# Kernel tuning notes

Hardware: AMD Instinct MI355X
Metric: run time of the kernel (lower is better)

Reference implementation:

```python
import jax, jax.numpy as jnp
import numpy as np

DIM = 1024
HEADS = 16
HEAD_DIM = DIM // HEADS


def setup_inputs() -> dict:
    key = jax.random.key(0)
    ks = jax.random.split(key, 10)
    B, N, M = 4, 2048, 2048
    s = 1.0 / np.sqrt(DIM)
    return {
        "x": jax.random.normal(ks[0], (B, N, DIM), jnp.float32),
        "context": jax.random.normal(ks[1], (B, M, DIM), jnp.float32),
        "Wq": jax.random.normal(ks[2], (DIM, DIM), jnp.float32) * s,
        "bq": jnp.zeros((DIM,), jnp.float32),
        "Wk": jax.random.normal(ks[3], (DIM, DIM), jnp.float32) * s,
        "bk": jnp.zeros((DIM,), jnp.float32),
        "Wv": jax.random.normal(ks[4], (DIM, DIM), jnp.float32) * s,
        "bv": jnp.zeros((DIM,), jnp.float32),
        "Wo": jax.random.normal(ks[5], (DIM, DIM), jnp.float32) * s,
        "bo": jnp.zeros((DIM,), jnp.float32),
    }


def reference(x, context, Wq, bq, Wk, bk, Wv, bv, Wo, bo):
    B, N, C = x.shape
    M = context.shape[1]
    scale = HEAD_DIM ** (-0.5)
    # projections + split heads: [B, H, L, D]
    q = (x @ Wq.T + bq).reshape(B, N, HEADS, HEAD_DIM).transpose(0, 2, 1, 3)
    k = (context @ Wk.T + bk).reshape(B, M, HEADS, HEAD_DIM).transpose(0, 2, 1, 3)
    v = (context @ Wv.T + bv).reshape(B, M, HEADS, HEAD_DIM).transpose(0, 2, 1, 3)
    attn = jax.nn.softmax(jnp.einsum('bhnd,bhmd->bhnm', q, k) * scale, axis=-1)
    out = jnp.einsum('bhnm,bhmd->bhnd', attn, v)  # [B, H, N, D]
    out = out.transpose(0, 2, 1, 3).reshape(B, N, C)
    return out @ Wo.T + bo
```

## Files before the change

kernel.cpp:

```cpp
#include <hip/hip_runtime.h>
#include <hip/hip_bf16.h>
#include <stdint.h>


#define HEADS 16
#define HD 64
#define NSEQ 2048
#define DIMSZ 1024

typedef __bf16 bf16x8_t __attribute__((ext_vector_type(8)));
typedef float f32x4_t __attribute__((ext_vector_type(4)));
typedef short s16x4 __attribute__((ext_vector_type(4)));
typedef unsigned short u16;
typedef unsigned int u32;

__device__ __forceinline__ u16 f2bf(float f) {
    union { float f; u32 i; } x; x.f = f;
    u32 r = x.i + 0x7FFF + ((x.i >> 16) & 1);
    return (u16)(r >> 16);
}
__device__ __forceinline__ u32 pk2(float a, float b) {
    __hip_bfloat162 h = __float22bfloat162_rn(float2{a, b});
    union { __hip_bfloat162 h2; u32 u; } c; c.h2 = h; return c.u;
}

__device__ __forceinline__ void pl32swap(u32& a, u32& b) {
    asm("v_permlane32_swap_b32 %0, %1" : "+v"(a), "+v"(b));
}
__device__ __forceinline__ void pl16swap(u32& a, u32& b) {
    asm("v_permlane16_swap_b32 %0, %1" : "+v"(a), "+v"(b));
}

#define GLDS(g, l) __builtin_amdgcn_global_load_lds( \
    (const __attribute__((address_space(1))) void*)(g), \
    (__attribute__((address_space(3))) void*)(l), 16, 0, 0)

__global__ __launch_bounds__(256)
void cvt_all(const float* __restrict__ x, const float* __restrict__ ctx,
             const float* __restrict__ wq, const float* __restrict__ wk,
             const float* __restrict__ wv, const float* __restrict__ wo,
             u16* __restrict__ xb, u16* __restrict__ ctxb,
             u16* __restrict__ wqb, u16* __restrict__ wkb,
             u16* __restrict__ wvb, u16* __restrict__ wob)
{
    long g = (long)blockIdx.x * 256 + threadIdx.x;
    const float* in; u16* out; long off;
    if (g < 1048576L)      { in = x;   out = xb;   off = g; }
    else if (g < 2097152L) { in = ctx; out = ctxb; off = g - 1048576L; }
    else if (g < 2228224L) { in = wq;  out = wqb;  off = g - 2097152L; }
    else if (g < 2359296L) { in = wk;  out = wkb;  off = g - 2228224L; }
    else if (g < 2490368L) { in = wv;  out = wvb;  off = g - 2359296L; }
    else                   { in = wo;  out = wob;  off = g - 2490368L; }
    long i = off * 8;
    float4 a = *(const float4*)(in + i);
    float4 b = *(const float4*)(in + i + 4);
    union { uint4 v; u16 h[8]; } u;
    u.h[0] = f2bf(a.x); u.h[1] = f2bf(a.y); u.h[2] = f2bf(a.z); u.h[3] = f2bf(a.w);
    u.h[4] = f2bf(b.x); u.h[5] = f2bf(b.y); u.h[6] = f2bf(b.z); u.h[7] = f2bf(b.w);
    *(uint4*)(out + i) = u.v;
}

#define BM 128
#define BN 128

#define BKQ 64

__global__ __launch_bounds__(256, 3)
void qkv_gemm(const u16* __restrict__ xb, const u16* __restrict__ ctxb,
              const u16* __restrict__ wq, const u16* __restrict__ wk,
              const u16* __restrict__ wv,
              const float* __restrict__ bq, const float* __restrict__ bk,
              const float* __restrict__ bv,
              u16* __restrict__ qo, u16* __restrict__ ko, u16* __restrict__ vo,
              float qscale)
{
    __shared__ __align__(16) u16 Asm[BM * BKQ];
    __shared__ __align__(16) u16 Wsm[BN * BKQ];

    const int g    = blockIdx.x >> 3;
    const int col0 = (blockIdx.x & 7) * BN;
    const int row0 = blockIdx.y * BM;

    const u16* A = (g == 0) ? xb : ctxb;
    const u16* W = (g == 0) ? wq : (g == 1) ? wk : wv;
    const float* bias = (g == 0) ? bq : (g == 1) ? bk : bv;
    const float scale = (g == 0) ? qscale : 1.0f;

    const int t    = threadIdx.x;
    const int lane = t & 63;
    const int wid  = t >> 6;
    const int lrow = lane & 15;
    const int lq   = lane >> 4;
    const int wm   = (wid >> 1) * 64;
    const int wn   = (wid & 1) * 64;

    const u16* gA[4]; const u16* gW[4];
    u16* lA[4]; u16* lW[4];
    #pragma unroll
    for (int q = 0; q < 4; q++) {
        int s = q * 256 + t;
        int r = s >> 3;
        int c = (s & 7) ^ (r & 7);
        gA[q] = A + (long)(row0 + r) * DIMSZ + c * 8;
        gW[q] = W + (long)(col0 + r) * DIMSZ + c * 8;
        int lofs = (q * 256 + wid * 64) * 8;
        lA[q] = &Asm[lofs];
        lW[q] = &Wsm[lofs];
    }

    f32x4_t zero = {0.f, 0.f, 0.f, 0.f};
    f32x4_t acc[4][4];
    #pragma unroll
    for (int i = 0; i < 4; i++)
        #pragma unroll
        for (int j = 0; j < 4; j++) acc[i][j] = zero;

    const int rsw = lrow & 7;

    for (int k0 = 0; k0 < DIMSZ; k0 += BKQ) {
        __syncthreads();
        #pragma unroll
        for (int q = 0; q < 4; q++) {
            GLDS(gA[q] + k0, lA[q]);
            GLDS(gW[q] + k0, lW[q]);
        }
        __syncthreads();

        #pragma unroll
        for (int kk = 0; kk < 2; kk++) {
            bf16x8_t af[4], bfr[4];
            #pragma unroll
            for (int i = 0; i < 4; i++)
                af[i] = *(const bf16x8_t*)
                    &Asm[(wm + 16 * i + lrow) * BKQ + (((kk * 4 + lq) ^ rsw) << 3)];
            #pragma unroll
            for (int j = 0; j < 4; j++)
                bfr[j] = *(const bf16x8_t*)
                    &Wsm[(wn + 16 * j + lrow) * BKQ + (((kk * 4 + lq) ^ rsw) << 3)];
            #pragma unroll
            for (int i = 0; i < 4; i++)
                #pragma unroll
                for (int j = 0; j < 4; j++)
                    acc[i][j] = __builtin_amdgcn_mfma_f32_16x16x32_bf16(
                        af[i], bfr[j], acc[i][j], 0, 0, 0);
        }
    }

    float bvv[4];
    #pragma unroll
    for (int j = 0; j < 4; j++) bvv[j] = bias[col0 + wn + 16 * j + lrow];

    if (g < 2) {
        u16* out = g ? ko : qo;
        #pragma unroll
        for (int i = 0; i < 4; i++) {
            #pragma unroll
            for (int j = 0; j < 4; j++) {
                int cc = col0 + wn + 16 * j + lrow;
                #pragma unroll
                for (int r = 0; r < 4; r++) {
                    int rr = row0 + wm + 16 * i + lq * 4 + r;
                    float v = (acc[i][j][r] + bvv[j]) * scale;
                    int b = rr >> 11, n = rr & 2047;
                    int h = cc >> 6,  d = cc & 63;
                    long oidx = ((long)((b * HEADS + h) * NSEQ + n) << 6) + d;
                    out[oidx] = f2bf(v);
                }
            }
        }
    } else {
        #pragma unroll
        for (int i = 0; i < 4; i++) {
            int n0 = row0 + wm + 16 * i + lq * 4;
            int b  = n0 >> 11, nn = n0 & 2047;
            #pragma unroll
            for (int j = 0; j < 4; j++) {
                int d = col0 + wn + 16 * j + lrow;
                uint2 p;
                p.x = pk2(acc[i][j][0] + bvv[j], acc[i][j][1] + bvv[j]);
                p.y = pk2(acc[i][j][2] + bvv[j], acc[i][j][3] + bvv[j]);
                long o = ((long)((b * HEADS + (d >> 6)) * HD + (d & 63)) << 11) + nn;
                *(uint2*)&vo[o] = p;
            }
        }
    }
}

#define BMO 64
#define BKO 64

__global__ __launch_bounds__(256, 4)
void gemm_o(const u16* __restrict__ A, const u16* __restrict__ W,
            const float* __restrict__ bias, float* __restrict__ out)
{
    __shared__ __align__(16) u16 Asm[BMO * BKO];
    __shared__ __align__(16) u16 Wsm[BN * BKO];

    const int t    = threadIdx.x;
    const int lane = t & 63;
    const int wid  = t >> 6;
    const int lrow = lane & 15;
    const int lq   = lane >> 4;
    const int wm   = (wid >> 1) * 32;
    const int wn   = (wid & 1) * 64;
    const int row0 = blockIdx.y * BMO;
    const int col0 = blockIdx.x * BN;

    const u16* gA[2]; u16* lA[2];
    #pragma unroll
    for (int q = 0; q < 2; q++) {
        int s = q * 256 + t;
        int r = s >> 3;
        int c = (s & 7) ^ (r & 7);
        gA[q] = A + (long)(row0 + r) * DIMSZ + c * 8;
        lA[q] = &Asm[(q * 256 + wid * 64) * 8];
    }
    const u16* gW[4]; u16* lW[4];
    #pragma unroll
    for (int q = 0; q < 4; q++) {
        int s = q * 256 + t;
        int r = s >> 3;
        int c = (s & 7) ^ (r & 7);
        gW[q] = W + (long)(col0 + r) * DIMSZ + c * 8;
        lW[q] = &Wsm[(q * 256 + wid * 64) * 8];
    }

    f32x4_t zero = {0.f, 0.f, 0.f, 0.f};
    f32x4_t acc[2][4];
    #pragma unroll
    for (int i = 0; i < 2; i++)
        #pragma unroll
        for (int j = 0; j < 4; j++) acc[i][j] = zero;

    const int rsw = lrow & 7;

    for (int k0 = 0; k0 < DIMSZ; k0 += BKO) {
        __syncthreads();
        GLDS(gA[0] + k0, lA[0]);
        GLDS(gA[1] + k0, lA[1]);
        #pragma unroll
        for (int q = 0; q < 4; q++) GLDS(gW[q] + k0, lW[q]);
        __syncthreads();

        #pragma unroll
        for (int kk = 0; kk < 2; kk++) {
            bf16x8_t af[2], bfr[4];
            #pragma unroll
            for (int i = 0; i < 2; i++)
                af[i] = *(const bf16x8_t*)
                    &Asm[(wm + 16 * i + lrow) * BKO + (((kk * 4 + lq) ^ rsw) << 3)];
            #pragma unroll
            for (int j = 0; j < 4; j++)
                bfr[j] = *(const bf16x8_t*)
                    &Wsm[(wn + 16 * j + lrow) * BKO + (((kk * 4 + lq) ^ rsw) << 3)];
            #pragma unroll
            for (int i = 0; i < 2; i++)
                #pragma unroll
                for (int j = 0; j < 4; j++)
                    acc[i][j] = __builtin_amdgcn_mfma_f32_16x16x32_bf16(
                        af[i], bfr[j], acc[i][j], 0, 0, 0);
        }
    }

    float bvv[4];
    #pragma unroll
    for (int j = 0; j < 4; j++) bvv[j] = bias[col0 + wn + 16 * j + lrow];

    #pragma unroll
    for (int i = 0; i < 2; i++) {
        #pragma unroll
        for (int j = 0; j < 4; j++) {
            int cc = col0 + wn + 16 * j + lrow;
            #pragma unroll
            for (int r = 0; r < 4; r++) {
                int rr = row0 + wm + 16 * i + lq * 4 + r;
                out[(long)rr * DIMSZ + cc] = acc[i][j][r] + bvv[j];
            }
        }
    }
}

__global__ __launch_bounds__(256, 4)
void attn(const u16* __restrict__ Q, const u16* __restrict__ K,
          const u16* __restrict__ Vt, u16* __restrict__ O)
{
    __shared__ __align__(16) u16 Ksm[2][64 * 64];
    __shared__ __align__(16) u16 Vsm[2][64 * 64];

    const int t    = threadIdx.x;
    const int lane = t & 63;
    const int w    = t >> 6;
    const int lrow = lane & 15;
    const int lq   = lane >> 4;
    const int bh   = blockIdx.x;
    const int q0   = blockIdx.y * 128;
    const int b    = bh >> 4;
    const int h    = bh & 15;

    bf16x8_t qf[2][2];
    #pragma unroll
    for (int qa = 0; qa < 2; qa++) {
        const long qbase = ((long)bh * NSEQ + q0 + w * 32 + qa * 16 + lrow) * HD;
        qf[qa][0] = *(const bf16x8_t*)&Q[qbase + lq * 8];
        qf[qa][1] = *(const bf16x8_t*)&Q[qbase + lq * 8 + 32];
    }

    const long kvbase = (long)bh * NSEQ * HD;

    const u16* gK[2]; const u16* gV[2]; int lofs[2];
    #pragma unroll
    for (int c = 0; c < 2; c++) {
        int s  = c * 256 + t;
        int r  = s >> 3;
        int ch = (s & 7) ^ (r & 7);
        gK[c] = K  + kvbase + (long)r * HD + ch * 8;
        gV[c] = Vt + kvbase + (long)r * NSEQ + ch * 8;
        lofs[c] = (c * 256 + w * 64) * 8;
    }

    f32x4_t zero = {0.f, 0.f, 0.f, 0.f};
    f32x4_t oacc[2][4];
    #pragma unroll
    for (int qa = 0; qa < 2; qa++)
        #pragma unroll
        for (int jd = 0; jd < 4; jd++) oacc[qa][jd] = zero;
    f32x4_t lacc[2] = {zero, zero};

    union { u32 u[4]; bf16x8_t v; } ob;
    ob.u[0] = ob.u[1] = ob.u[2] = ob.u[3] = 0x3F803F80u;
    const bf16x8_t onesb = ob.v;

    const int rsw = lrow & 7;

    auto stage = [&](int ktn, int nb) {
        long ko = (long)ktn * (64 * HD);
        int  vo = ktn * 64;
        GLDS(gK[0] + ko, &Ksm[nb][lofs[0]]);
        GLDS(gK[1] + ko, &Ksm[nb][lofs[1]]);
        GLDS(gV[0] + vo, &Vsm[nb][lofs[0]]);
        GLDS(gV[1] + vo, &Vsm[nb][lofs[1]]);
    };

    auto tile = [&](const u16* Ks, const u16* Vs) {
        f32x4_t sacc[2][4];
        #pragma unroll
        for (int jt = 0; jt < 4; jt++) {
            sacc[0][jt] = zero; sacc[1][jt] = zero;
            #pragma unroll
            for (int kk = 0; kk < 2; kk++) {
                bf16x8_t kf = *(const bf16x8_t*)
                    &Ks[(16 * jt + lrow) * 64 + (((kk * 4 + lq) ^ rsw) << 3)];
                sacc[0][jt] = __builtin_amdgcn_mfma_f32_16x16x32_bf16(
                    kf, qf[0][kk], sacc[0][jt], 0, 0, 0);
                sacc[1][jt] = __builtin_amdgcn_mfma_f32_16x16x32_bf16(
                    kf, qf[1][kk], sacc[1][jt], 0, 0, 0);
            }
        }

        bf16x8_t pa32[2][2];
        #pragma unroll
        for (int qa = 0; qa < 2; qa++) {
            #pragma unroll
            for (int t2 = 0; t2 < 2; t2++) {
                u32 uu[2][2];
                #pragma unroll
                for (int half = 0; half < 2; half++) {
                    int jt = t2 * 2 + half;
                    float p0 = exp2f(sacc[qa][jt][0]);
                    float p1 = exp2f(sacc[qa][jt][1]);
                    float p2 = exp2f(sacc[qa][jt][2]);
                    float p3 = exp2f(sacc[qa][jt][3]);
                    uu[half][0] = pk2(p0, p1);
                    uu[half][1] = pk2(p2, p3);
                }
                pl32swap(uu[0][0], uu[1][0]);
                pl16swap(uu[0][0], uu[1][0]);
                pl32swap(uu[0][1], uu[1][1]);
                pl16swap(uu[0][1], uu[1][1]);
                union { u32 u[4]; bf16x8_t v; } pk_;
                pk_.u[0] = uu[0][0]; pk_.u[1] = uu[0][1];
                pk_.u[2] = uu[1][0]; pk_.u[3] = uu[1][1];
                pa32[qa][t2] = pk_.v;
                lacc[qa] = __builtin_amdgcn_mfma_f32_16x16x32_bf16(
                    pa32[qa][t2], onesb, lacc[qa], 0, 0, 0);
            }
        }

        #pragma unroll
        for (int jd = 0; jd < 4; jd++) {
            #pragma unroll
            for (int t2 = 0; t2 < 2; t2++) {
                bf16x8_t vb = *(const bf16x8_t*)
                    &Vs[(16 * jd + lrow) * 64 + (((4 * t2 + lq) ^ rsw) << 3)];
                oacc[0][jd] = __builtin_amdgcn_mfma_f32_16x16x32_bf16(
                    pa32[0][t2], vb, oacc[0][jd], 0, 0, 0);
                oacc[1][jd] = __builtin_amdgcn_mfma_f32_16x16x32_bf16(
                    pa32[1][t2], vb, oacc[1][jd], 0, 0, 0);
            }
        }
    };

    stage(0, 0);
    __syncthreads();

    for (int kt = 0; kt < NSEQ / 64; kt += 2) {
        stage(kt + 1, 1);
        tile(Ksm[0], Vsm[0]);
        __syncthreads();
        if (kt + 2 < NSEQ / 64) stage(kt + 2, 0);
        tile(Ksm[1], Vsm[1]);
        __syncthreads();
    }

    float linv[2][4];
    #pragma unroll
    for (int qa = 0; qa < 2; qa++)
        #pragma unroll
        for (int r = 0; r < 4; r++)
            linv[qa][r] = __builtin_amdgcn_rcpf(lacc[qa][r]);

    #pragma unroll
    for (int qa = 0; qa < 2; qa++) {
        #pragma unroll
        for (int jd = 0; jd < 4; jd++) {
            #pragma unroll
            for (int r = 0; r < 4; r++) {
                int qrow = q0 + w * 32 + qa * 16 + lq * 4 + r;
                int d    = 16 * jd + lrow;
                long oidx = ((long)(b * NSEQ + qrow)) * DIMSZ + h * HD + d;
                O[oidx] = f2bf(oacc[qa][jd][r] * linv[qa][r]);
            }
        }
    }
}

extern "C" void kernel_launch(void* const* d_in, const int* in_sizes, int n_in,
                              void* d_out, int out_size, void* d_ws, size_t ws_size,
                              hipStream_t stream)
{
    const float* x   = (const float*)d_in[0];
    const float* ctx = (const float*)d_in[1];
    const float* Wq  = (const float*)d_in[2];
    const float* bq  = (const float*)d_in[3];
    const float* Wk  = (const float*)d_in[4];
    const float* bk  = (const float*)d_in[5];
    const float* Wv  = (const float*)d_in[6];
    const float* bv  = (const float*)d_in[7];
    const float* Wo  = (const float*)d_in[8];
    const float* bo  = (const float*)d_in[9];
    float* out = (float*)d_out;

    const size_t NX = (size_t)8192 * 1024;
    const size_t NW = (size_t)1024 * 1024;

    u16* xb   = (u16*)d_ws;
    u16* ctxb = xb + NX;
    u16* wqb  = ctxb + NX;
    u16* wkb  = wqb + NW;
    u16* wvb  = wkb + NW;
    u16* wob  = wvb + NW;
    u16* qws  = wob + NW;
    u16* kws  = qws + NX;
    u16* vws  = kws + NX;
    u16* aws  = xb;

    cvt_all<<<10240, 256, 0, stream>>>(x, ctx, Wq, Wk, Wv, Wo,
                                       xb, ctxb, wqb, wkb, wvb, wob);

    const float qscale = 0.125f * 1.44269504088896340736f;

    qkv_gemm<<<dim3(24, 8192 / BM), 256, 0, stream>>>(
        xb, ctxb, wqb, wkb, wvb, bq, bk, bv, qws, kws, vws, qscale);
    attn<<<dim3(64, NSEQ / 128), 256, 0, stream>>>(qws, kws, vws, aws);
    gemm_o<<<dim3(DIMSZ / BN, 8192 / BMO), 256, 0, stream>>>(aws, wob, bo, out);
}
```

Measured before the change: 342.5 us.

## Enlarge output GEMM tile and interleave attention QK/softmax/PV per half-tile

The output projection GEMM now uses the same BM row tile as the QKV GEMM (128 rows, 64x64 per wave), which doubles A reuse and halves the number of blocks, with occupancy lowered to 3. The attention inner loop is reorganized to compute scores, exponentiate and accumulate PV per 32-key half, and it adds s_setprio around the MFMA sections so matrix work is prioritized over other waves' exp work. exp2f is replaced with the hardware builtin exp2 when available. Costs include higher register pressure in gemm_o, fewer blocks for load balance, and slightly less precise exp.

```diff
diff --git a/kernel.cpp b/kernel.cpp
--- a/kernel.cpp
+++ b/kernel.cpp
@@ -23,6 +23,15 @@
     __hip_bfloat162 h = __float22bfloat162_rn(float2{a, b});
     union { __hip_bfloat162 h2; u32 u; } c; c.h2 = h; return c.u;
 }
+
+#if defined(__has_builtin)
+#if __has_builtin(__builtin_amdgcn_exp2f)
+#define EXP2(x) __builtin_amdgcn_exp2f(x)
+#endif
+#endif
+#ifndef EXP2
+#define EXP2(x) exp2f(x)
+#endif
 
 __device__ __forceinline__ void pl32swap(u32& a, u32& b) {
     asm("v_permlane32_swap_b32 %0, %1" : "+v"(a), "+v"(b));
@@ -186,14 +195,13 @@
     }
 }
 
-#define BMO 64
 #define BKO 64
 
-__global__ __launch_bounds__(256, 4)
+__global__ __launch_bounds__(256, 3)
 void gemm_o(const u16* __restrict__ A, const u16* __restrict__ W,
             const float* __restrict__ bias, float* __restrict__ out)
 {
-    __shared__ __align__(16) u16 Asm[BMO * BKO];
+    __shared__ __align__(16) u16 Asm[BM * BKO];
     __shared__ __align__(16) u16 Wsm[BN * BKO];
 
     const int t    = threadIdx.x;
@@ -201,34 +209,29 @@
     const int wid  = t >> 6;
     const int lrow = lane & 15;
     const int lq   = lane >> 4;
-    const int wm   = (wid >> 1) * 32;
+    const int wm   = (wid >> 1) * 64;
     const int wn   = (wid & 1) * 64;
-    const int row0 = blockIdx.y * BMO;
+    const int row0 = blockIdx.y * BM;
     const int col0 = blockIdx.x * BN;
 
-    const u16* gA[2]; u16* lA[2];
-    #pragma unroll
-    for (int q = 0; q < 2; q++) {
+    const u16* gA[4]; const u16* gW[4];
+    u16* lA[4]; u16* lW[4];
+    #pragma unroll
+    for (int q = 0; q < 4; q++) {
         int s = q * 256 + t;
         int r = s >> 3;
         int c = (s & 7) ^ (r & 7);
         gA[q] = A + (long)(row0 + r) * DIMSZ + c * 8;
-        lA[q] = &Asm[(q * 256 + wid * 64) * 8];
-    }
-    const u16* gW[4]; u16* lW[4];
-    #pragma unroll
-    for (int q = 0; q < 4; q++) {
-        int s = q * 256 + t;
-        int r = s >> 3;
-        int c = (s & 7) ^ (r & 7);
         gW[q] = W + (long)(col0 + r) * DIMSZ + c * 8;
-        lW[q] = &Wsm[(q * 256 + wid * 64) * 8];
+        int lofs = (q * 256 + wid * 64) * 8;
+        lA[q] = &Asm[lofs];
+        lW[q] = &Wsm[lofs];
     }
 
     f32x4_t zero = {0.f, 0.f, 0.f, 0.f};
-    f32x4_t acc[2][4];
-    #pragma unroll
-    for (int i = 0; i < 2; i++)
+    f32x4_t acc[4][4];
+    #pragma unroll
+    for (int i = 0; i < 4; i++)
         #pragma unroll
         for (int j = 0; j < 4; j++) acc[i][j] = zero;
 
@@ -236,17 +239,18 @@
 
     for (int k0 = 0; k0 < DIMSZ; k0 += BKO) {
         __syncthreads();
-        GLDS(gA[0] + k0, lA[0]);
-        GLDS(gA[1] + k0, lA[1]);
-        #pragma unroll
-        for (int q = 0; q < 4; q++) GLDS(gW[q] + k0, lW[q]);
+        #pragma unroll
+        for (int q = 0; q < 4; q++) {
+            GLDS(gA[q] + k0, lA[q]);
+            GLDS(gW[q] + k0, lW[q]);
+        }
         __syncthreads();
 
         #pragma unroll
         for (int kk = 0; kk < 2; kk++) {
-            bf16x8_t af[2], bfr[4];
-            #pragma unroll
-            for (int i = 0; i < 2; i++)
+            bf16x8_t af[4], bfr[4];
+            #pragma unroll
+            for (int i = 0; i < 4; i++)
                 af[i] = *(const bf16x8_t*)
                     &Asm[(wm + 16 * i + lrow) * BKO + (((kk * 4 + lq) ^ rsw) << 3)];
             #pragma unroll
@@ -254,7 +258,7 @@
                 bfr[j] = *(const bf16x8_t*)
                     &Wsm[(wn + 16 * j + lrow) * BKO + (((kk * 4 + lq) ^ rsw) << 3)];
             #pragma unroll
-            for (int i = 0; i < 2; i++)
+            for (int i = 0; i < 4; i++)
                 #pragma unroll
                 for (int j = 0; j < 4; j++)
                     acc[i][j] = __builtin_amdgcn_mfma_f32_16x16x32_bf16(
@@ -267,7 +271,7 @@
     for (int j = 0; j < 4; j++) bvv[j] = bias[col0 + wn + 16 * j + lrow];
 
     #pragma unroll
-    for (int i = 0; i < 2; i++) {
+    for (int i = 0; i < 4; i++) {
         #pragma unroll
         for (int j = 0; j < 4; j++) {
             int cc = col0 + wn + 16 * j + lrow;
@@ -342,36 +346,40 @@
     };
 
     auto tile = [&](const u16* Ks, const u16* Vs) {
-        f32x4_t sacc[2][4];
-        #pragma unroll
-        for (int jt = 0; jt < 4; jt++) {
-            sacc[0][jt] = zero; sacc[1][jt] = zero;
-            #pragma unroll
-            for (int kk = 0; kk < 2; kk++) {
-                bf16x8_t kf = *(const bf16x8_t*)
-                    &Ks[(16 * jt + lrow) * 64 + (((kk * 4 + lq) ^ rsw) << 3)];
-                sacc[0][jt] = __builtin_amdgcn_mfma_f32_16x16x32_bf16(
-                    kf, qf[0][kk], sacc[0][jt], 0, 0, 0);
-                sacc[1][jt] = __builtin_amdgcn_mfma_f32_16x16x32_bf16(
-                    kf, qf[1][kk], sacc[1][jt], 0, 0, 0);
-            }
-        }
-
-        bf16x8_t pa32[2][2];
-        #pragma unroll
-        for (int qa = 0; qa < 2; qa++) {
-            #pragma unroll
-            for (int t2 = 0; t2 < 2; t2++) {
+        #pragma unroll
+        for (int t2 = 0; t2 < 2; t2++) {
+            f32x4_t sacc[2][2];
+            __builtin_amdgcn_s_setprio(1);
+            #pragma unroll
+            for (int jh = 0; jh < 2; jh++) {
+                int jt = t2 * 2 + jh;
+                bf16x8_t kf0 = *(const bf16x8_t*)
+                    &Ks[(16 * jt + lrow) * 64 + ((lq ^ rsw) << 3)];
+                bf16x8_t kf1 = *(const bf16x8_t*)
+                    &Ks[(16 * jt + lrow) * 64 + (((4 + lq) ^ rsw) << 3)];
+                sacc[jh][0] = __builtin_amdgcn_mfma_f32_16x16x32_bf16(
+                    kf0, qf[0][0], zero, 0, 0, 0);
+                sacc[jh][1] = __builtin_amdgcn_mfma_f32_16x16x32_bf16(
+                    kf0, qf[1][0], zero, 0, 0, 0);
+                sacc[jh][0] = __builtin_amdgcn_mfma_f32_16x16x32_bf16(
+                    kf1, qf[0][1], sacc[jh][0], 0, 0, 0);
+                sacc[jh][1] = __builtin_amdgcn_mfma_f32_16x16x32_bf16(
+                    kf1, qf[1][1], sacc[jh][1], 0, 0, 0);
+            }
+            __builtin_amdgcn_s_setprio(0);
+
+            bf16x8_t pa32[2];
+            #pragma unroll
+            for (int qa = 0; qa < 2; qa++) {
                 u32 uu[2][2];
                 #pragma unroll
-                for (int half = 0; half < 2; half++) {
-                    int jt = t2 * 2 + half;
-                    float p0 = exp2f(sacc[qa][jt][0]);
-                    float p1 = exp2f(sacc[qa][jt][1]);
-                    float p2 = exp2f(sacc[qa][jt][2]);
-                    float p3 = exp2f(sacc[qa][jt][3]);
-                    uu[half][0] = pk2(p0, p1);
-                    uu[half][1] = pk2(p2, p3);
+                for (int jh = 0; jh < 2; jh++) {
+                    float p0 = EXP2(sacc[jh][qa][0]);
+                    float p1 = EXP2(sacc[jh][qa][1]);
+                    float p2 = EXP2(sacc[jh][qa][2]);
+                    float p3 = EXP2(sacc[jh][qa][3]);
+                    uu[jh][0] = pk2(p0, p1);
+                    uu[jh][1] = pk2(p2, p3);
                 }
                 pl32swap(uu[0][0], uu[1][0]);
                 pl16swap(uu[0][0], uu[1][0]);
@@ -380,23 +388,24 @@
                 union { u32 u[4]; bf16x8_t v; } pk_;
                 pk_.u[0] = uu[0][0]; pk_.u[1] = uu[0][1];
                 pk_.u[2] = uu[1][0]; pk_.u[3] = uu[1][1];
-                pa32[qa][t2] = pk_.v;
-                lacc[qa] = __builtin_amdgcn_mfma_f32_16x16x32_bf16(
-                    pa32[qa][t2], onesb, lacc[qa], 0, 0, 0);
-            }
-        }
-
-        #pragma unroll
-        for (int jd = 0; jd < 4; jd++) {
-            #pragma unroll
-            for (int t2 = 0; t2 < 2; t2++) {
+                pa32[qa] = pk_.v;
+            }
+
+            __builtin_amdgcn_s_setprio(1);
+            lacc[0] = __builtin_amdgcn_mfma_f32_16x16x32_bf16(
+                pa32[0], onesb, lacc[0], 0, 0, 0);
+            lacc[1] = __builtin_amdgcn_mfma_f32_16x16x32_bf16(
+                pa32[1], onesb, lacc[1], 0, 0, 0);
+            #pragma unroll
+            for (int jd = 0; jd < 4; jd++) {
                 bf16x8_t vb = *(const bf16x8_t*)
                     &Vs[(16 * jd + lrow) * 64 + (((4 * t2 + lq) ^ rsw) << 3)];
                 oacc[0][jd] = __builtin_amdgcn_mfma_f32_16x16x32_bf16(
-                    pa32[0][t2], vb, oacc[0][jd], 0, 0, 0);
+                    pa32[0], vb, oacc[0][jd], 0, 0, 0);
                 oacc[1][jd] = __builtin_amdgcn_mfma_f32_16x16x32_bf16(
-                    pa32[1][t2], vb, oacc[1][jd], 0, 0, 0);
-            }
+                    pa32[1], vb, oacc[1][jd], 0, 0, 0);
+            }
+            __builtin_amdgcn_s_setprio(0);
         }
     };
 
@@ -472,5 +481,5 @@
     qkv_gemm<<<dim3(24, 8192 / BM), 256, 0, stream>>>(
         xb, ctxb, wqb, wkb, wvb, bq, bk, bv, qws, kws, vws, qscale);
     attn<<<dim3(64, NSEQ / 128), 256, 0, stream>>>(qws, kws, vws, aws);
-    gemm_o<<<dim3(DIMSZ / BN, 8192 / BMO), 256, 0, stream>>>(aws, wob, bo, out);
-}
+    gemm_o<<<dim3(DIMSZ / BN, 8192 / BM), 256, 0, stream>>>(aws, wob, bo, out);
+}
```

After: 312.4 us. 1.1x faster.
